# Optimization experiments

Measured on AMD Instinct MI355X. Metric: run time of the kernel, lower is better.

Reference implementation:

```python
import jax, jax.numpy as jnp
import numpy as np

N_NODES = 50000
N_EDGES = 800000
IN_CH = 128
OUT_CH = 32
HEADS = 8
NEG_SLOPE = 0.2


def setup_inputs() -> dict:
    key = jax.random.key(0)
    k1, k2, k3, k4, k5, k6 = jax.random.split(key, 6)
    x = jax.random.normal(k1, (N_NODES, IN_CH), dtype=jnp.float32)
    edge_index = jax.random.randint(k2, (2, N_EDGES), 0, N_NODES, dtype=jnp.int64)
    # Glorot-ish scaled params
    W = jax.random.normal(k3, (IN_CH, HEADS * OUT_CH), dtype=jnp.float32) * (1.0 / np.sqrt(IN_CH))
    att_src = jax.random.normal(k4, (HEADS, OUT_CH), dtype=jnp.float32) * (1.0 / np.sqrt(OUT_CH))
    att_dst = jax.random.normal(k5, (HEADS, OUT_CH), dtype=jnp.float32) * (1.0 / np.sqrt(OUT_CH))
    bias = jax.random.normal(k6, (HEADS * OUT_CH,), dtype=jnp.float32) * 0.01
    return {"x": x, "edge_index": edge_index, "W": W, "att_src": att_src, "att_dst": att_dst, "bias": bias}


def reference(x, edge_index, W, att_src, att_dst, bias):
    N = x.shape[0]
    # PyG GATConv default: add self loops
    loops = jnp.arange(N, dtype=edge_index.dtype)
    src = jnp.concatenate([edge_index[0], loops])  # message source j
    dst = jnp.concatenate([edge_index[1], loops])  # message destination i

    # Linear projection: [N, H, C]
    h = (x @ W).reshape(N, HEADS, OUT_CH)

    # Per-node attention logits per head: [N, H]
    a_src = jnp.einsum('nhc,hc->nh', h, att_src)
    a_dst = jnp.einsum('nhc,hc->nh', h, att_dst)

    # Per-edge scores: [E, H]
    e = jax.nn.leaky_relu(a_src[src] + a_dst[dst], NEG_SLOPE)

    # Segment softmax over edges sharing a destination (self loops guarantee non-empty segments)
    e_max = jax.ops.segment_max(e, dst, num_segments=N)
    e_exp = jnp.exp(e - e_max[dst])
    e_sum = jax.ops.segment_sum(e_exp, dst, num_segments=N)
    alpha = e_exp / (e_sum[dst] + 1e-16)  # [E, H]

    # Weighted message aggregation: [N, H, C] -> concat heads [N, H*C]
    msg = h[src] * alpha[:, :, None]
    out = jax.ops.segment_sum(msg, dst, num_segments=N).reshape(N, HEADS * OUT_CH)
    out = out + bias
    # unlinear = ReLU (act='relu', norm=None)
    return jax.nn.relu(out)
```

## Files before the change

### kernel.cpp

```cpp
#include <hip/hip_runtime.h>

#define IN_CH 128
#define OUT_CH 32
#define HEADS 8
#define HC 256
#define NEG_SLOPE 0.2f

typedef __attribute__((ext_vector_type(8))) short short8;
typedef __attribute__((ext_vector_type(4))) float f32x4;

__device__ __forceinline__ float bflo(unsigned u) { return __uint_as_float(u << 16); }
__device__ __forceinline__ float bfhi(unsigned u) { return __uint_as_float(u & 0xffff0000u); }
__device__ __forceinline__ float bf2f(unsigned short u) { return __uint_as_float(((unsigned)u) << 16); }
__device__ __forceinline__ unsigned short f2bf(float f) {
    unsigned u = __float_as_uint(f);
    u = (u + 0x7fffu + ((u >> 16) & 1u)) >> 16;
    return (unsigned short)u;
}

__global__ __launch_bounds__(256)
void gat_prep(const float* __restrict__ W, unsigned short* __restrict__ Wt,
              int* __restrict__ counts, int n)
{
    const int idx = blockIdx.x * 256 + threadIdx.x;
    const int k = idx >> 8;
    const int col = idx & 255;
    Wt[col * IN_CH + k] = f2bf(W[idx]);
    for (int i = idx; i < n; i += 32768) counts[i] = 0;
}

__global__ __launch_bounds__(256)
void gat_proj_mfma(const float* __restrict__ x, const unsigned short* __restrict__ Wt,
                   const float* __restrict__ attS, const float* __restrict__ attD,
                   unsigned short* __restrict__ h, float* __restrict__ aS,
                   float* __restrict__ aD, int N)
{
    __shared__ unsigned short xs[32 * 136];

    const int tid = threadIdx.x;
    const int lane = tid & 63;
    const int w = tid >> 6;
    const int row0 = blockIdx.x * 32;

    short8 bfr[4][4];
    {
        const unsigned short* wp = Wt + (size_t)(w * 64 + (lane & 15)) * IN_CH
                                      + ((lane >> 4) << 3);
#pragma unroll
        for (int i = 0; i < 4; ++i)
#pragma unroll
            for (int ks = 0; ks < 4; ++ks)
                bfr[ks][i] = *(const short8*)(wp + i * 16 * IN_CH + ks * 32);
    }

#pragma unroll
    for (int u = 0; u < 2; ++u) {
        const int unit = tid + u * 256;
        const int srow = unit >> 4;
        const int sseg = unit & 15;
        const int grow = row0 + srow;
        float4 v0 = make_float4(0.f, 0.f, 0.f, 0.f), v1 = v0;
        if (grow < N) {
            const float* xp = x + (size_t)grow * IN_CH + sseg * 8;
            v0 = *(const float4*)xp;
            v1 = *(const float4*)(xp + 4);
        }
        unsigned short* lp = xs + srow * 136 + sseg * 8;
        lp[0] = f2bf(v0.x); lp[1] = f2bf(v0.y); lp[2] = f2bf(v0.z); lp[3] = f2bf(v0.w);
        lp[4] = f2bf(v1.x); lp[5] = f2bf(v1.y); lp[6] = f2bf(v1.z); lp[7] = f2bf(v1.w);
    }
    __syncthreads();

    f32x4 acc[2][4];
#pragma unroll
    for (int m = 0; m < 2; ++m)
#pragma unroll
        for (int i = 0; i < 4; ++i) acc[m][i] = (f32x4){0.f, 0.f, 0.f, 0.f};

#pragma unroll
    for (int ks = 0; ks < 4; ++ks) {
#pragma unroll
        for (int m = 0; m < 2; ++m) {
            const short8 a = *(const short8*)&xs[((lane & 15) + m * 16) * 136
                                                 + ks * 32 + ((lane >> 4) << 3)];
#pragma unroll
            for (int i = 0; i < 4; ++i)
                acc[m][i] = __builtin_amdgcn_mfma_f32_16x16x32_bf16(a, bfr[ks][i], acc[m][i], 0, 0, 0);
        }
    }

    const int rbase = (lane >> 4) << 2;
    float ps[2][2][4], pd[2][2][4];
#pragma unroll
    for (int m = 0; m < 2; ++m)
#pragma unroll
        for (int hp = 0; hp < 2; ++hp)
#pragma unroll
            for (int r = 0; r < 4; ++r) { ps[m][hp][r] = 0.f; pd[m][hp][r] = 0.f; }

#pragma unroll
    for (int i = 0; i < 4; ++i) {
        const int col = w * 64 + i * 16 + (lane & 15);
        const int hp = i >> 1;
        const float asv = attS[(w * 2 + hp) * 32 + (i & 1) * 16 + (lane & 15)];
        const float adv = attD[(w * 2 + hp) * 32 + (i & 1) * 16 + (lane & 15)];
#pragma unroll
        for (int m = 0; m < 2; ++m) {
#pragma unroll
            for (int r = 0; r < 4; ++r) {
                const int grow = row0 + m * 16 + rbase + r;
                if (grow < N) h[(size_t)grow * HC + col] = f2bf(acc[m][i][r]);
                ps[m][hp][r] = fmaf(acc[m][i][r], asv, ps[m][hp][r]);
                pd[m][hp][r] = fmaf(acc[m][i][r], adv, pd[m][hp][r]);
            }
        }
    }
#pragma unroll
    for (int off = 1; off < 16; off <<= 1) {
#pragma unroll
        for (int m = 0; m < 2; ++m)
#pragma unroll
            for (int hp = 0; hp < 2; ++hp)
#pragma unroll
                for (int r = 0; r < 4; ++r) {
                    ps[m][hp][r] += __shfl_xor(ps[m][hp][r], off, 64);
                    pd[m][hp][r] += __shfl_xor(pd[m][hp][r], off, 64);
                }
    }
    if ((lane & 15) == 0) {
#pragma unroll
        for (int m = 0; m < 2; ++m)
#pragma unroll
            for (int hp = 0; hp < 2; ++hp)
#pragma unroll
                for (int r = 0; r < 4; ++r) {
                    const int grow = row0 + m * 16 + rbase + r;
                    if (grow < N) {
                        aS[grow * HEADS + w * 2 + hp] = ps[m][hp][r];
                        aD[grow * HEADS + w * 2 + hp] = pd[m][hp][r];
                    }
                }
    }
}

__global__ __launch_bounds__(256)
void gat_hist(const int* __restrict__ dst, int* __restrict__ counts, int E)
{
    int i = (blockIdx.x * 256 + threadIdx.x) * 4;
    if (i + 3 < E) {
        const int4 d = *(const int4*)&dst[i];
        atomicAdd(&counts[d.x], 1);
        atomicAdd(&counts[d.y], 1);
        atomicAdd(&counts[d.z], 1);
        atomicAdd(&counts[d.w], 1);
    } else {
        for (; i < E; ++i) atomicAdd(&counts[dst[i]], 1);
    }
}

__global__ __launch_bounds__(256)
void gat_scan1(const int* __restrict__ counts, int* __restrict__ bsum, int n)
{
    __shared__ int ws[4];
    const int t = threadIdx.x;
    const int lane = t & 63;
    const int wid = t >> 6;
    const int idx = blockIdx.x * 1024 + t * 4;
    int4 v = {0, 0, 0, 0};
    if (idx + 3 < n) v = *(const int4*)&counts[idx];
    else {
        if (idx < n)     v.x = counts[idx];
        if (idx + 1 < n) v.y = counts[idx + 1];
        if (idx + 2 < n) v.z = counts[idx + 2];
    }
    int s4 = v.x + v.y + v.z + v.w;
#pragma unroll
    for (int off = 1; off < 64; off <<= 1) s4 += __shfl_xor(s4, off, 64);
    if (lane == 0) ws[wid] = s4;
    __syncthreads();
    if (t == 0) bsum[blockIdx.x] = ws[0] + ws[1] + ws[2] + ws[3];
}

__global__ __launch_bounds__(256)
void gat_scan3(const int* __restrict__ counts, const int* __restrict__ bsum,
               int* __restrict__ offsets, int* __restrict__ cursor,
               int n, int nb, int E)
{
    __shared__ int wsums[4];
    __shared__ int bbase_s;
    const int t = threadIdx.x;
    const int lane = t & 63;
    const int wid = t >> 6;

    if (t < 64) {
        const int v = (t < nb) ? bsum[t] : 0;
        int inc = v;
#pragma unroll
        for (int off = 1; off < 64; off <<= 1) {
            const int y = __shfl_up(inc, off, 64);
            if (t >= off) inc += y;
        }
        const int myv   = __shfl(v, blockIdx.x, 64);
        const int myinc = __shfl(inc, blockIdx.x, 64);
        if (t == 0) bbase_s = myinc - myv;
    }

    const int idx = blockIdx.x * 1024 + t * 4;
    int4 v = {0, 0, 0, 0};
    if (idx + 3 < n) v = *(const int4*)&counts[idx];
    else {
        if (idx < n)     v.x = counts[idx];
        if (idx + 1 < n) v.y = counts[idx + 1];
        if (idx + 2 < n) v.z = counts[idx + 2];
    }
    const int s4 = v.x + v.y + v.z + v.w;
    int inc = s4;
#pragma unroll
    for (int off = 1; off < 64; off <<= 1) {
        const int y = __shfl_up(inc, off, 64);
        if (lane >= off) inc += y;
    }
    if (lane == 63) wsums[wid] = inc;
    __syncthreads();
    int wbase = 0;
    for (int i = 0; i < wid; ++i) wbase += wsums[i];
    const int base = bbase_s + wbase + (inc - s4);
    int4 o;
    o.x = base;
    o.y = base + v.x;
    o.z = o.y + v.y;
    o.w = o.z + v.z;
    if (idx + 3 < n) {
        *(int4*)&offsets[idx] = o;
        *(int4*)&cursor[idx] = o;
    } else {
        if (idx < n)     { offsets[idx] = o.x;     cursor[idx] = o.x; }
        if (idx + 1 < n) { offsets[idx + 1] = o.y; cursor[idx + 1] = o.y; }
        if (idx + 2 < n) { offsets[idx + 2] = o.z; cursor[idx + 2] = o.z; }
    }
    if (blockIdx.x == 0 && t == 0) offsets[n] = E;
}

__global__ __launch_bounds__(256)
void gat_scatter(const int* __restrict__ src, const int* __restrict__ dst,
                 int* __restrict__ cursor, int* __restrict__ ssrc,
                 unsigned short* __restrict__ ealpha,
                 const float* __restrict__ aS, const float* __restrict__ aD, int E)
{
    const int e = blockIdx.x * 256 + threadIdx.x;
    if (e >= E) return;
    const int s = src[e];
    const int d = dst[e];
    const int pos = atomicAdd(&cursor[d], 1);
    ssrc[pos] = s;
    const float4 s0 = *(const float4*)(aS + (size_t)s * HEADS);
    const float4 s1 = *(const float4*)(aS + (size_t)s * HEADS + 4);
    const float4 d0 = *(const float4*)(aD + (size_t)d * HEADS);
    const float4 d1 = *(const float4*)(aD + (size_t)d * HEADS + 4);
    float lg[8] = { s0.x + d0.x, s0.y + d0.y, s0.z + d0.z, s0.w + d0.w,
                    s1.x + d1.x, s1.y + d1.y, s1.z + d1.z, s1.w + d1.w };
    short8 al;
#pragma unroll
    for (int k = 0; k < 8; ++k) {
        const float v = lg[k] > 0.f ? lg[k] : NEG_SLOPE * lg[k];
        al[k] = (short)f2bf(__expf(v));
    }
    *(short8*)(ealpha + (size_t)pos * HEADS) = al;
}

__global__ __launch_bounds__(256)
void gat_agg(const unsigned short* __restrict__ h,
             const float* __restrict__ aS, const float* __restrict__ aD,
             const int* __restrict__ offsets, const int* __restrict__ ssrc,
             const unsigned short* __restrict__ ealpha,
             const float* __restrict__ bias, float* __restrict__ out, int N)
{
    const int t = threadIdx.x;
    const int lane = t & 63;
    const int node = blockIdx.x * 4 + (t >> 6);
    if (node >= N) return;

    const int half = lane >> 5;
    const int hl = lane & 31;
    const int head = hl >> 2;
    const int ch = head * 32 + (hl & 3) * 8;

    float sum;
    float acc[8];
    {
        float lg0 = aS[node * HEADS + head] + aD[node * HEADS + head];
        lg0 = (lg0 > 0.f) ? lg0 : NEG_SLOPE * lg0;
        const float w0 = half ? 0.f : __expf(lg0);
        sum = w0;
        const uint4 hv = *(const uint4*)(h + (size_t)node * HC + ch);
        acc[0] = w0 * bflo(hv.x); acc[1] = w0 * bfhi(hv.x);
        acc[2] = w0 * bflo(hv.y); acc[3] = w0 * bfhi(hv.y);
        acc[4] = w0 * bflo(hv.z); acc[5] = w0 * bfhi(hv.z);
        acc[6] = w0 * bflo(hv.w); acc[7] = w0 * bfhi(hv.w);
    }

    const int beg = offsets[node];
    const int end = offsets[node + 1];
    const int last = end - 1;

    int sE[4];
    float aE[4];
#pragma unroll
    for (int j = 0; j < 4; ++j) { sE[j] = node; aE[j] = 0.f; }

    if (beg < end) {
#pragma unroll
        for (int j = 0; j < 4; ++j) {
            const int e = beg + half * 4 + j;
            const int c = min(e, last);
            int s = ssrc[c];
            float a = bf2f(ealpha[(size_t)c * HEADS + head]);
            if (e > last) { s = node; a = 0.f; }
            sE[j] = s; aE[j] = a;
        }
    }

    for (int base = beg; base < end; base += 8) {
        int tS[4]; float tA[4];
#pragma unroll
        for (int j = 0; j < 4; ++j) {
            const int e = base + 8 + half * 4 + j;
            const int c = min(e, last);
            int s = ssrc[c];
            float a = bf2f(ealpha[(size_t)c * HEADS + head]);
            if (e > last) { s = node; a = 0.f; }
            tS[j] = s; tA[j] = a;
        }
        uint4 v[4];
#pragma unroll
        for (int j = 0; j < 4; ++j)
            v[j] = *(const uint4*)(h + (size_t)sE[j] * HC + ch);
#pragma unroll
        for (int j = 0; j < 4; ++j) {
            const float a = aE[j];
            sum += a;
            acc[0] = fmaf(a, bflo(v[j].x), acc[0]);
            acc[1] = fmaf(a, bfhi(v[j].x), acc[1]);
            acc[2] = fmaf(a, bflo(v[j].y), acc[2]);
            acc[3] = fmaf(a, bfhi(v[j].y), acc[3]);
            acc[4] = fmaf(a, bflo(v[j].z), acc[4]);
            acc[5] = fmaf(a, bfhi(v[j].z), acc[5]);
            acc[6] = fmaf(a, bflo(v[j].w), acc[6]);
            acc[7] = fmaf(a, bfhi(v[j].w), acc[7]);
        }
#pragma unroll
        for (int j = 0; j < 4; ++j) { sE[j] = tS[j]; aE[j] = tA[j]; }
    }

#pragma unroll
    for (int j = 0; j < 8; ++j) acc[j] += __shfl_xor(acc[j], 32, 64);
    sum += __shfl_xor(sum, 32, 64);

    const float inv = 1.f / (sum + 1e-16f);
    const int cbase = ch + half * 4;
    const int j0 = half * 4;
    const float4 bv = *(const float4*)(bias + cbase);
    float4 o;
    o.x = fmaxf(fmaf(acc[j0 + 0], inv, bv.x), 0.f);
    o.y = fmaxf(fmaf(acc[j0 + 1], inv, bv.y), 0.f);
    o.z = fmaxf(fmaf(acc[j0 + 2], inv, bv.z), 0.f);
    o.w = fmaxf(fmaf(acc[j0 + 3], inv, bv.w), 0.f);
    *(float4*)(out + (size_t)node * HC + cbase) = o;
}

extern "C" void kernel_launch(void* const* d_in, const int* in_sizes, int n_in,
                              void* d_out, int out_size, void* d_ws, size_t ws_size,
                              hipStream_t stream)
{
    const float* x    = (const float*)d_in[0];
    const int*   ei   = (const int*)d_in[1];
    const float* W    = (const float*)d_in[2];
    const float* attS = (const float*)d_in[3];
    const float* attD = (const float*)d_in[4];
    const float* bias = (const float*)d_in[5];
    float* out = (float*)d_out;

    const int N = in_sizes[0] / IN_CH;
    const int E = in_sizes[1] / 2;
    const int* esrc = ei;
    const int* edst = ei + E;

    unsigned short* h = (unsigned short*)d_ws;
    float* aS = (float*)(h + (size_t)N * HC);
    float* aD = aS + (size_t)N * HEADS;
    int* counts  = (int*)(aD + (size_t)N * HEADS);
    int* offsets = counts + N;
    int* cursor  = offsets + (N + 4);
    int* ssrc    = cursor + N;
    int* bsum    = ssrc + E;
    unsigned short* Wt = (unsigned short*)(bsum + 64);
    unsigned short* ealpha = Wt + IN_CH * HC;

    const int nb = (N + 1023) / 1024;

    gat_prep<<<(IN_CH * HC) / 256, 256, 0, stream>>>(W, Wt, counts, N);
    gat_proj_mfma<<<(N + 31) / 32, 256, 0, stream>>>(x, Wt, attS, attD, h, aS, aD, N);
    gat_hist<<<(E / 4 + 255) / 256, 256, 0, stream>>>(edst, counts, E);
    gat_scan1<<<nb, 256, 0, stream>>>(counts, bsum, N);
    gat_scan3<<<nb, 256, 0, stream>>>(counts, bsum, offsets, cursor, N, nb, E);
    gat_scatter<<<(E + 255) / 256, 256, 0, stream>>>(esrc, edst, cursor, ssrc, ealpha, aS, aD, E);
    gat_agg<<<(N + 3) / 4, 256, 0, stream>>>(h, aS, aD, offsets, ssrc, ealpha, bias, out, N);
}
```

Baseline: 190.0 us.

## Fuse CSR-building kernels into one cooperative kernel and coalesce projection stores

```diff
diff --git a/kernel.cpp b/kernel.cpp
--- a/kernel.cpp
+++ b/kernel.cpp
@@ -1,4 +1,7 @@
 #include <hip/hip_runtime.h>
+#include <hip/hip_cooperative_groups.h>
+
+namespace cg = cooperative_groups;
 
 #define IN_CH 128
 #define OUT_CH 32
@@ -19,14 +22,106 @@
 }
 
 __global__ __launch_bounds__(256)
-void gat_prep(const float* __restrict__ W, unsigned short* __restrict__ Wt,
-              int* __restrict__ counts, int n)
+void gat_csr(const float* __restrict__ W, unsigned short* __restrict__ Wt,
+             const int* __restrict__ dst, int* __restrict__ counts,
+             int* __restrict__ bsum, int* __restrict__ offsets,
+             int* __restrict__ cursor, int N, int E, int nb)
 {
-    const int idx = blockIdx.x * 256 + threadIdx.x;
-    const int k = idx >> 8;
-    const int col = idx & 255;
-    Wt[col * IN_CH + k] = f2bf(W[idx]);
-    for (int i = idx; i < n; i += 32768) counts[i] = 0;
+    cg::grid_group grid = cg::this_grid();
+    __shared__ int ws[4];
+    __shared__ int bbase_s;
+
+    const int tid = threadIdx.x;
+    const int gid = blockIdx.x * 256 + tid;
+    const int gs = gridDim.x * 256;
+    const int lane = tid & 63;
+    const int wid = tid >> 6;
+
+    for (int idx = gid; idx < IN_CH * HC; idx += gs) {
+        const int k = idx >> 8;
+        const int col = idx & 255;
+        Wt[col * IN_CH + k] = f2bf(W[idx]);
+    }
+    for (int i = gid; i < N; i += gs) counts[i] = 0;
+    grid.sync();
+
+    const int nquads = E >> 2;
+    for (int q = gid; q < nquads; q += gs) {
+        const int4 d = *(const int4*)&dst[q * 4];
+        atomicAdd(&counts[d.x], 1);
+        atomicAdd(&counts[d.y], 1);
+        atomicAdd(&counts[d.z], 1);
+        atomicAdd(&counts[d.w], 1);
+    }
+    if (gid < (E & 3)) atomicAdd(&counts[nquads * 4 + gid < N ? dst[nquads * 4 + gid] : 0], 1);
+    grid.sync();
+
+    if (blockIdx.x < (unsigned)nb) {
+        const int idx = blockIdx.x * 1024 + tid * 4;
+        int4 v = {0, 0, 0, 0};
+        if (idx + 3 < N) v = *(const int4*)&counts[idx];
+        else {
+            if (idx < N)     v.x = counts[idx];
+            if (idx + 1 < N) v.y = counts[idx + 1];
+            if (idx + 2 < N) v.z = counts[idx + 2];
+        }
+        int s4 = v.x + v.y + v.z + v.w;
+#pragma unroll
+        for (int off = 1; off < 64; off <<= 1) s4 += __shfl_xor(s4, off, 64);
+        if (lane == 0) ws[wid] = s4;
+        __syncthreads();
+        if (tid == 0) bsum[blockIdx.x] = ws[0] + ws[1] + ws[2] + ws[3];
+    }
+    grid.sync();
+
+    if (blockIdx.x < (unsigned)nb) {
+        if (tid < 64) {
+            const int v = (tid < nb) ? bsum[tid] : 0;
+            int inc = v;
+#pragma unroll
+            for (int off = 1; off < 64; off <<= 1) {
+                const int y = __shfl_up(inc, off, 64);
+                if (tid >= off) inc += y;
+            }
+            const int myv   = __shfl(v, blockIdx.x, 64);
+            const int myinc = __shfl(inc, blockIdx.x, 64);
+            if (tid == 0) bbase_s = myinc - myv;
+        }
+        const int idx = blockIdx.x * 1024 + tid * 4;
+        int4 v = {0, 0, 0, 0};
+        if (idx + 3 < N) v = *(const int4*)&counts[idx];
+        else {
+            if (idx < N)     v.x = counts[idx];
+            if (idx + 1 < N) v.y = counts[idx + 1];
+            if (idx + 2 < N) v.z = counts[idx + 2];
+        }
+        const int s4 = v.x + v.y + v.z + v.w;
+        int inc = s4;
+#pragma unroll
+        for (int off = 1; off < 64; off <<= 1) {
+            const int y = __shfl_up(inc, off, 64);
+            if (lane >= off) inc += y;
+        }
+        if (lane == 63) ws[wid] = inc;
+        __syncthreads();
+        int wbase = 0;
+        for (int i = 0; i < wid; ++i) wbase += ws[i];
+        const int base = bbase_s + wbase + (inc - s4);
+        int4 o;
+        o.x = base;
+        o.y = base + v.x;
+        o.z = o.y + v.y;
+        o.w = o.z + v.z;
+        if (idx + 3 < N) {
+            *(int4*)&offsets[idx] = o;
+            *(int4*)&cursor[idx] = o;
+        } else {
+            if (idx < N)     { offsets[idx] = o.x;     cursor[idx] = o.x; }
+            if (idx + 1 < N) { offsets[idx + 1] = o.y; cursor[idx + 1] = o.y; }
+            if (idx + 2 < N) { offsets[idx + 2] = o.z; cursor[idx + 2] = o.z; }
+        }
+        if (blockIdx.x == 0 && tid == 0) offsets[N] = E;
+    }
 }
 
 __global__ __launch_bounds__(256)
@@ -35,7 +130,7 @@
                    unsigned short* __restrict__ h, float* __restrict__ aS,
                    float* __restrict__ aD, int N)
 {
-    __shared__ unsigned short xs[32 * 136];
+    __shared__ unsigned short lbuf[32 * 264];
 
     const int tid = threadIdx.x;
     const int lane = tid & 63;
@@ -65,9 +160,12 @@
             v0 = *(const float4*)xp;
             v1 = *(const float4*)(xp + 4);
         }
-        unsigned short* lp = xs + srow * 136 + sseg * 8;
-        lp[0] = f2bf(v0.x); lp[1] = f2bf(v0.y); lp[2] = f2bf(v0.z); lp[3] = f2bf(v0.w);
-        lp[4] = f2bf(v1.x); lp[5] = f2bf(v1.y); lp[6] = f2bf(v1.z); lp[7] = f2bf(v1.w);
+        short8 pk;
+        pk[0] = (short)f2bf(v0.x); pk[1] = (short)f2bf(v0.y);
+        pk[2] = (short)f2bf(v0.z); pk[3] = (short)f2bf(v0.w);
+        pk[4] = (short)f2bf(v1.x); pk[5] = (short)f2bf(v1.y);
+        pk[6] = (short)f2bf(v1.z); pk[7] = (short)f2bf(v1.w);
+        *(short8*)&lbuf[srow * 136 + sseg * 8] = pk;
     }
     __syncthreads();
 
@@ -81,8 +179,8 @@
     for (int ks = 0; ks < 4; ++ks) {
 #pragma unroll
         for (int m = 0; m < 2; ++m) {
-            const short8 a = *(const short8*)&xs[((lane & 15) + m * 16) * 136
-                                                 + ks * 32 + ((lane >> 4) << 3)];
+            const short8 a = *(const short8*)&lbuf[((lane & 15) + m * 16) * 136
+                                                   + ks * 32 + ((lane >> 4) << 3)];
 #pragma unroll
             for (int i = 0; i < 4; ++i)
                 acc[m][i] = __builtin_amdgcn_mfma_f32_16x16x32_bf16(a, bfr[ks][i], acc[m][i], 0, 0, 0);
@@ -100,20 +198,16 @@
 
 #pragma unroll
     for (int i = 0; i < 4; ++i) {
-        const int col = w * 64 + i * 16 + (lane & 15);
         const int hp = i >> 1;
         const float asv = attS[(w * 2 + hp) * 32 + (i & 1) * 16 + (lane & 15)];
         const float adv = attD[(w * 2 + hp) * 32 + (i & 1) * 16 + (lane & 15)];
 #pragma unroll
-        for (int m = 0; m < 2; ++m) {
+        for (int m = 0; m < 2; ++m)
 #pragma unroll
             for (int r = 0; r < 4; ++r) {
-                const int grow = row0 + m * 16 + rbase + r;
-                if (grow < N) h[(size_t)grow * HC + col] = f2bf(acc[m][i][r]);
                 ps[m][hp][r] = fmaf(acc[m][i][r], asv, ps[m][hp][r]);
                 pd[m][hp][r] = fmaf(acc[m][i][r], adv, pd[m][hp][r]);
             }
-        }
     }
 #pragma unroll
     for (int off = 1; off < 16; off <<= 1) {
@@ -141,104 +235,29 @@
                     }
                 }
     }
-}
-
-__global__ __launch_bounds__(256)
-void gat_hist(const int* __restrict__ dst, int* __restrict__ counts, int E)
-{
-    int i = (blockIdx.x * 256 + threadIdx.x) * 4;
-    if (i + 3 < E) {
-        const int4 d = *(const int4*)&dst[i];
-        atomicAdd(&counts[d.x], 1);
-        atomicAdd(&counts[d.y], 1);
-        atomicAdd(&counts[d.z], 1);
-        atomicAdd(&counts[d.w], 1);
-    } else {
-        for (; i < E; ++i) atomicAdd(&counts[dst[i]], 1);
-    }
-}
-
-__global__ __launch_bounds__(256)
-void gat_scan1(const int* __restrict__ counts, int* __restrict__ bsum, int n)
-{
-    __shared__ int ws[4];
-    const int t = threadIdx.x;
-    const int lane = t & 63;
-    const int wid = t >> 6;
-    const int idx = blockIdx.x * 1024 + t * 4;
-    int4 v = {0, 0, 0, 0};
-    if (idx + 3 < n) v = *(const int4*)&counts[idx];
-    else {
-        if (idx < n)     v.x = counts[idx];
-        if (idx + 1 < n) v.y = counts[idx + 1];
-        if (idx + 2 < n) v.z = counts[idx + 2];
-    }
-    int s4 = v.x + v.y + v.z + v.w;
-#pragma unroll
-    for (int off = 1; off < 64; off <<= 1) s4 += __shfl_xor(s4, off, 64);
-    if (lane == 0) ws[wid] = s4;
+
     __syncthreads();
-    if (t == 0) bsum[blockIdx.x] = ws[0] + ws[1] + ws[2] + ws[3];
-}
-
-__global__ __launch_bounds__(256)
-void gat_scan3(const int* __restrict__ counts, const int* __restrict__ bsum,
-               int* __restrict__ offsets, int* __restrict__ cursor,
-               int n, int nb, int E)
-{
-    __shared__ int wsums[4];
-    __shared__ int bbase_s;
-    const int t = threadIdx.x;
-    const int lane = t & 63;
-    const int wid = t >> 6;
-
-    if (t < 64) {
-        const int v = (t < nb) ? bsum[t] : 0;
-        int inc = v;
-#pragma unroll
-        for (int off = 1; off < 64; off <<= 1) {
-            const int y = __shfl_up(inc, off, 64);
-            if (t >= off) inc += y;
-        }
-        const int myv   = __shfl(v, blockIdx.x, 64);
-        const int myinc = __shfl(inc, blockIdx.x, 64);
-        if (t == 0) bbase_s = myinc - myv;
-    }
-
-    const int idx = blockIdx.x * 1024 + t * 4;
-    int4 v = {0, 0, 0, 0};
-    if (idx + 3 < n) v = *(const int4*)&counts[idx];
-    else {
-        if (idx < n)     v.x = counts[idx];
-        if (idx + 1 < n) v.y = counts[idx + 1];
-        if (idx + 2 < n) v.z = counts[idx + 2];
-    }
-    const int s4 = v.x + v.y + v.z + v.w;
-    int inc = s4;
-#pragma unroll
-    for (int off = 1; off < 64; off <<= 1) {
-        const int y = __shfl_up(inc, off, 64);
-        if (lane >= off) inc += y;
-    }
-    if (lane == 63) wsums[wid] = inc;
+#pragma unroll
+    for (int i = 0; i < 4; ++i) {
+        const int col = w * 64 + i * 16 + (lane & 15);
+#pragma unroll
+        for (int m = 0; m < 2; ++m)
+#pragma unroll
+            for (int r = 0; r < 4; ++r)
+                lbuf[(m * 16 + rbase + r) * 264 + col] = f2bf(acc[m][i][r]);
+    }
     __syncthreads();
-    int wbase = 0;
-    for (int i = 0; i < wid; ++i) wbase += wsums[i];
-    const int base = bbase_s + wbase + (inc - s4);
-    int4 o;
-    o.x = base;
-    o.y = base + v.x;
-    o.z = o.y + v.y;
-    o.w = o.z + v.z;
-    if (idx + 3 < n) {
-        *(int4*)&offsets[idx] = o;
-        *(int4*)&cursor[idx] = o;
-    } else {
-        if (idx < n)     { offsets[idx] = o.x;     cursor[idx] = o.x; }
-        if (idx + 1 < n) { offsets[idx + 1] = o.y; cursor[idx + 1] = o.y; }
-        if (idx + 2 < n) { offsets[idx + 2] = o.z; cursor[idx + 2] = o.z; }
-    }
-    if (blockIdx.x == 0 && t == 0) offsets[n] = E;
+
+#pragma unroll
+    for (int u = 0; u < 4; ++u) {
+        const int unit = u * 256 + tid;
+        const int srow = unit >> 5;
+        const int sseg = unit & 31;
+        const int grow = row0 + srow;
+        if (grow < N)
+            *(short8*)(h + (size_t)grow * HC + sseg * 8) =
+                *(const short8*)&lbuf[srow * 264 + sseg * 8];
+    }
 }
 
 __global__ __launch_bounds__(256)
@@ -380,8 +399,8 @@
     const float* bias = (const float*)d_in[5];
     float* out = (float*)d_out;
 
-    const int N = in_sizes[0] / IN_CH;
-    const int E = in_sizes[1] / 2;
+    int N = in_sizes[0] / IN_CH;
+    int E = in_sizes[1] / 2;
     const int* esrc = ei;
     const int* edst = ei + E;
 
@@ -396,13 +415,16 @@
     unsigned short* Wt = (unsigned short*)(bsum + 64);
     unsigned short* ealpha = Wt + IN_CH * HC;
 
-    const int nb = (N + 1023) / 1024;
-
-    gat_prep<<<(IN_CH * HC) / 256, 256, 0, stream>>>(W, Wt, counts, N);
+    int nb = (N + 1023) / 1024;
+
+    {
+        void* kargs[] = { (void*)&W, (void*)&Wt, (void*)&edst, (void*)&counts,
+                          (void*)&bsum, (void*)&offsets, (void*)&cursor,
+                          (void*)&N, (void*)&E, (void*)&nb };
+        hipLaunchCooperativeKernel((void*)gat_csr, dim3(256), dim3(256),
+                                   kargs, 0, stream);
+    }
     gat_proj_mfma<<<(N + 31) / 32, 256, 0, stream>>>(x, Wt, attS, attD, h, aS, aD, N);
-    gat_hist<<<(E / 4 + 255) / 256, 256, 0, stream>>>(edst, counts, E);
-    gat_scan1<<<nb, 256, 0, stream>>>(counts, bsum, N);
-    gat_scan3<<<nb, 256, 0, stream>>>(counts, bsum, offsets, cursor, N, nb, E);
     gat_scatter<<<(E + 255) / 256, 256, 0, stream>>>(esrc, edst, cursor, ssrc, ealpha, aS, aD, E);
     gat_agg<<<(N + 3) / 4, 256, 0, stream>>>(h, aS, aD, offsets, ssrc, ealpha, bias, out, N);
 }
```

Result: slower. 276.7 us (+45.7%).
